# Optimization experiments

Measured on AMD Instinct MI355X. Metric: run time of the kernel, lower is better.

Reference implementation:

```python
import jax, jax.numpy as jnp
import numpy as np

H = 16
D = 1024
DH = D // H


def setup_inputs() -> dict:
    key = jax.random.key(0)
    ks = jax.random.split(key, 7)
    B, N = 4, 2048
    queries = jax.random.normal(ks[0], (B, N, D), dtype=jnp.float32)
    keys = jax.random.normal(ks[1], (B, N, D), dtype=jnp.float32)
    values = jax.random.normal(ks[2], (B, N, D), dtype=jnp.float32)
    s = 1.0 / np.sqrt(D)
    Wq = jax.random.normal(ks[3], (D, D), dtype=jnp.float32) * s
    Wk = jax.random.normal(ks[4], (D, D), dtype=jnp.float32) * s
    Wv = jax.random.normal(ks[5], (D, D), dtype=jnp.float32) * s
    Wo = jax.random.normal(ks[6], (D, D), dtype=jnp.float32) * s
    return {"queries": queries, "keys": keys, "values": values,
            "Wq": Wq, "Wk": Wk, "Wv": Wv, "Wo": Wo}


def reference(queries, keys, values, Wq, Wk, Wv, Wo):
    B, Nq, _ = queries.shape
    Nk = keys.shape[1]
    # torch Linear (no bias): y = x @ W.T
    q = (queries @ Wq.T).reshape(B, Nq, H, DH)
    k = (keys @ Wk.T).reshape(B, Nk, H, DH)
    v = (values @ Wv.T).reshape(B, Nk, H, DH)
    scale = 1.0 / jnp.sqrt(jnp.asarray(DH, dtype=q.dtype))
    scores = jnp.einsum("bqhd,bkhd->bhqk", q, k) * scale  # (B,H,Nq,Nk)
    attn = jax.nn.softmax(scores, axis=-1)
    ctx = jnp.einsum("bhqk,bkhd->bqhd", attn, v).reshape(B, Nq, D)
    return ctx @ Wo.T
```

## Files before the change

kernel.cpp:

```cpp
#include <hip/hip_runtime.h>
#include <hip/hip_bf16.h>
#include <stdint.h>

typedef short bf16x8 __attribute__((ext_vector_type(8)));
typedef float f32x4 __attribute__((ext_vector_type(4)));
typedef unsigned short u16;
typedef unsigned int u32;

#define MFMA(a, b, c) __builtin_amdgcn_mfma_f32_16x16x32_bf16(a, b, c, 0, 0, 0)

#if __has_builtin(__builtin_amdgcn_exp2f)
#define EXP2F(x) __builtin_amdgcn_exp2f(x)
#else
#define EXP2F(x) exp2f(x)
#endif
#if __has_builtin(__builtin_amdgcn_rcpf)
#define RCPF(x) __builtin_amdgcn_rcpf(x)
#else
#define RCPF(x) (1.0f / (x))
#endif

__device__ __forceinline__ u16 f2bf(float f) {
  u32 u = __builtin_bit_cast(u32, f);
  u += 0x7FFFu + ((u >> 16) & 1u);
  return (u16)(u >> 16);
}

__device__ __forceinline__ bf16x8 cvt8(const float* p) {
  const float4 f0 = *(const float4*)p;
  const float4 f1 = *(const float4*)(p + 4);
  bf16x8 r;
  r[0] = (short)f2bf(f0.x); r[1] = (short)f2bf(f0.y);
  r[2] = (short)f2bf(f0.z); r[3] = (short)f2bf(f0.w);
  r[4] = (short)f2bf(f1.x); r[5] = (short)f2bf(f1.y);
  r[6] = (short)f2bf(f1.z); r[7] = (short)f2bf(f1.w);
  return r;
}

__device__ __forceinline__ void async16(const u16* g, u16* l) {
  __builtin_amdgcn_global_load_lds(
      (const __attribute__((address_space(1))) void*)g,
      (__attribute__((address_space(3))) void*)l, 16, 0, 0);
}

__global__ __launch_bounds__(256) void cvt_qk(const float* __restrict__ xq,
                                              const float* __restrict__ xk,
                                              u16* __restrict__ dq,
                                              u16* __restrict__ dk) {
  int b = (int)blockIdx.x;
  const float* s;
  u16* d;
  if (b < 4096) { s = xq; d = dq; } else { s = xk; d = dk; b -= 4096; }
  const size_t off = (size_t)b * 2048 + (size_t)threadIdx.x * 8;
  *(bf16x8*)(d + off) = cvt8(s + off);
}

__global__ __launch_bounds__(256) void cvt_vw(
    const float* __restrict__ xv, const float* __restrict__ wq,
    const float* __restrict__ wk, const float* __restrict__ wv,
    const float* __restrict__ wo, u16* __restrict__ dv, u16* __restrict__ dwq,
    u16* __restrict__ dwk, u16* __restrict__ dwv, u16* __restrict__ dwo) {
  int b = (int)blockIdx.x;
  const float* s;
  u16* d;
  if (b < 4096) { s = xv; d = dv; }
  else if (b < 4608) { s = wq; d = dwq; b -= 4096; }
  else if (b < 5120) { s = wk; d = dwk; b -= 4608; }
  else if (b < 5632) { s = wv; d = dwv; b -= 5120; }
  else { s = wo; d = dwo; b -= 5632; }
  const size_t off = (size_t)b * 2048 + (size_t)threadIdx.x * 8;
  *(bf16x8*)(d + off) = cvt8(s + off);
}

__device__ __forceinline__ void gemm_core(const u16* __restrict__ A,
                                          const u16* __restrict__ W,
                                          u16* smA, u16* smB, f32x4 acc[4][4],
                                          int m0, int n0, int tid) {
  const int w = tid >> 6, l = tid & 63;
  const int la = l & 15, q = l >> 4;
  const int wm = w >> 1, wn = w & 1;
  const int srow = tid >> 3, sblk = tid & 7;

  for (int kk = 0; kk < 16; ++kk) {
    __syncthreads();
#pragma unroll
    for (int jj = 0; jj < 4; ++jj) {
      const int row = jj * 32 + srow;
      const int sb = (sblk ^ (row & 7)) * 8;
      const int ld = (jj * 256 + tid) * 8;
      async16(A + (size_t)(m0 + row) * 1024 + kk * 64 + sb, smA + ld);
      async16(W + (size_t)(n0 + row) * 1024 + kk * 64 + sb, smB + ld);
    }
    __syncthreads();
#pragma unroll
    for (int ks = 0; ks < 2; ++ks) {
      bf16x8 af[4], bfr[4];
#pragma unroll
      for (int im = 0; im < 4; ++im)
        af[im] = *(const bf16x8*)(smA + (wm * 64 + im * 16 + la) * 64 +
                                  (((ks * 4 + q) ^ (la & 7)) * 8));
#pragma unroll
      for (int in = 0; in < 4; ++in)
        bfr[in] = *(const bf16x8*)(smB + (wn * 64 + in * 16 + la) * 64 +
                                   (((ks * 4 + q) ^ (la & 7)) * 8));
#pragma unroll
      for (int im = 0; im < 4; ++im)
#pragma unroll
        for (int in = 0; in < 4; ++in)
          acc[im][in] = MFMA(af[im], bfr[in], acc[im][in]);
    }
  }
}

__global__ __launch_bounds__(256, 2) void gemm_qkv(
    const u16* __restrict__ Xqb, const u16* __restrict__ Xkb,
    const u16* __restrict__ Xvb, const u16* __restrict__ Wqb,
    const u16* __restrict__ Wkb, const u16* __restrict__ Wvb,
    u16* __restrict__ Qh, u16* __restrict__ Kh, u16* __restrict__ VTp) {
  __shared__ u16 smA[128 * 64];
  __shared__ u16 smB[128 * 64];
  const int z = (int)blockIdx.z;
  const u16* A = (z == 0) ? Xqb : (z == 1) ? Xkb : Xvb;
  const u16* W = (z == 0) ? Wqb : (z == 1) ? Wkb : Wvb;
  u16* out = (z == 0) ? Qh : (z == 1) ? Kh : VTp;
  const float scale = (z == 0) ? 0.18033688011112042f : 1.0f;

  const int tid = (int)threadIdx.x;
  const int w = tid >> 6, l = tid & 63;
  const int la = l & 15, q = l >> 4;
  const int m0 = blockIdx.x * 128, n0 = blockIdx.y * 128;
  const int wm = w >> 1, wn = w & 1;

  f32x4 acc[4][4];
#pragma unroll
  for (int i = 0; i < 4; ++i)
#pragma unroll
    for (int j = 0; j < 4; ++j) acc[i][j] = (f32x4){0.f, 0.f, 0.f, 0.f};

  gemm_core(A, W, smA, smB, acc, m0, n0, tid);

#pragma unroll
  for (int im = 0; im < 4; ++im) {
    const int mbase = m0 + wm * 64 + im * 16 + q * 4;
#pragma unroll
    for (int in = 0; in < 4; ++in) {
      const int n = n0 + wn * 64 + in * 16 + la;
      if (z == 2) {
        const int b = mbase >> 11, nr = mbase & 2047;
        const int h = n >> 6, d = n & 63;
        uint2 val;
        val.x = (u32)f2bf(acc[im][in][0]) | ((u32)f2bf(acc[im][in][1]) << 16);
        val.y = (u32)f2bf(acc[im][in][2]) | ((u32)f2bf(acc[im][in][3]) << 16);
        *(uint2*)(VTp + ((size_t)((b * 16 + h) * 64 + d)) * 2048 + nr) = val;
      } else {
#pragma unroll
        for (int r = 0; r < 4; ++r) {
          const int mm = mbase + r;
          const int b = mm >> 11, nr = mm & 2047;
          const int h = n >> 6, d = n & 63;
          out[((size_t)((b * 16 + h) * 2048 + nr)) * 64 + d] =
              f2bf(acc[im][in][r] * scale);
        }
      }
    }
  }
}

__global__ __launch_bounds__(256, 2) void gemm_out(const u16* __restrict__ A,
                                                   const u16* __restrict__ W,
                                                   float* __restrict__ out) {
  __shared__ u16 smA[128 * 64];
  __shared__ u16 smB[128 * 64];
  const int tid = (int)threadIdx.x;
  const int w = tid >> 6, l = tid & 63;
  const int la = l & 15, q = l >> 4;
  const int m0 = blockIdx.x * 128, n0 = blockIdx.y * 128;
  const int wm = w >> 1, wn = w & 1;

  f32x4 acc[4][4];
#pragma unroll
  for (int i = 0; i < 4; ++i)
#pragma unroll
    for (int j = 0; j < 4; ++j) acc[i][j] = (f32x4){0.f, 0.f, 0.f, 0.f};

  gemm_core(A, W, smA, smB, acc, m0, n0, tid);

#pragma unroll
  for (int im = 0; im < 4; ++im) {
    const int mbase = m0 + wm * 64 + im * 16 + q * 4;
#pragma unroll
    for (int in = 0; in < 4; ++in) {
      const int n = n0 + wn * 64 + in * 16 + la;
#pragma unroll
      for (int r = 0; r < 4; ++r)
        out[(size_t)(mbase + r) * 1024 + n] = acc[im][in][r];
    }
  }
}

__global__ __launch_bounds__(256, 2) void attn_kernel(const u16* __restrict__ Qh,
                                                      const u16* __restrict__ Kh,
                                                      const u16* __restrict__ VT,
                                                      u16* __restrict__ ctx) {
  __shared__ u16 smK[128 * 64];
  __shared__ u16 smV[64 * 128];
  __shared__ u16 smP[128 * 128];

  const int tid = (int)threadIdx.x;
  const int w = tid >> 6, l = tid & 63;
  const int la = l & 15, q = l >> 4;
  const int qt = blockIdx.x, bh = blockIdx.y;
  const u16* Qp = Qh + (size_t)bh * (2048 * 64);
  const u16* Kp = Kh + (size_t)bh * (2048 * 64);
  const u16* Vp = VT + (size_t)bh * (64 * 2048);

  bf16x8 qf[2][2];
#pragma unroll
  for (int ic = 0; ic < 2; ++ic)
#pragma unroll
    for (int ks = 0; ks < 2; ++ks)
      qf[ic][ks] = *(const bf16x8*)(Qp + (size_t)(qt * 128 + w * 32 + ic * 16 + la) * 64 +
                                    ks * 32 + q * 8);

  f32x4 accO[2][4];
#pragma unroll
  for (int ic = 0; ic < 2; ++ic)
#pragma unroll
    for (int dc = 0; dc < 4; ++dc) accO[ic][dc] = (f32x4){0.f, 0.f, 0.f, 0.f};
  float m_[2] = {-__builtin_inff(), -__builtin_inff()};
  float l_[2] = {0.f, 0.f};
  float alpha_[2];
  bool skip_[2];

  const int srow = tid >> 3, sblk = tid & 7;

  for (int kt = 0; kt < 16; ++kt) {
    __syncthreads();
#pragma unroll
    for (int jj = 0; jj < 4; ++jj) {
      const int idx = jj * 256 + tid;
      const int krow = jj * 32 + srow;
      const int ksb = (sblk ^ (krow & 7)) * 8;
      async16(Kp + (size_t)(kt * 128 + krow) * 64 + ksb, smK + idx * 8);
      const int vr = idx >> 4, vb = idx & 15;
      async16(Vp + (size_t)vr * 2048 + kt * 128 + ((vb ^ (vr & 15)) * 8),
              smV + idx * 8);
    }
    __syncthreads();

    f32x4 st[2][8];
#pragma unroll
    for (int ic = 0; ic < 2; ++ic)
#pragma unroll
      for (int jc = 0; jc < 8; ++jc) st[ic][jc] = (f32x4){0.f, 0.f, 0.f, 0.f};
    __builtin_amdgcn_s_setprio(1);
#pragma unroll
    for (int ks = 0; ks < 2; ++ks) {
      bf16x8 kf[8];
#pragma unroll
      for (int jc = 0; jc < 8; ++jc)
        kf[jc] = *(const bf16x8*)(smK + (jc * 16 + la) * 64 +
                                  (((ks * 4 + q) ^ (la & 7)) * 8));
#pragma unroll
      for (int jc = 0; jc < 8; ++jc)
#pragma unroll
        for (int ic = 0; ic < 2; ++ic)
          st[ic][jc] = MFMA(kf[jc], qf[ic][ks], st[ic][jc]);
    }
    __builtin_amdgcn_s_setprio(0);

#pragma unroll
    for (int ic = 0; ic < 2; ++ic) {
      float mx = -__builtin_inff();
#pragma unroll
      for (int jc = 0; jc < 8; ++jc)
#pragma unroll
        for (int r = 0; r < 4; ++r) mx = fmaxf(mx, st[ic][jc][r]);
      mx = fmaxf(mx, __shfl_xor(mx, 16));
      mx = fmaxf(mx, __shfl_xor(mx, 32));
      const bool skip = (bool)__all(mx - m_[ic] <= 8.0f);
      float mnew, al;
      if (skip) { mnew = m_[ic]; al = 1.0f; }
      else { mnew = fmaxf(m_[ic], mx); al = EXP2F(m_[ic] - mnew); }
      skip_[ic] = skip;
      alpha_[ic] = al;
      float rs = 0.f;
      const int i = w * 32 + ic * 16 + la;
#pragma unroll
      for (int jc = 0; jc < 8; ++jc) {
        const float p0 = EXP2F(st[ic][jc][0] - mnew);
        const float p1 = EXP2F(st[ic][jc][1] - mnew);
        const float p2 = EXP2F(st[ic][jc][2] - mnew);
        const float p3 = EXP2F(st[ic][jc][3] - mnew);
        rs += (p0 + p1) + (p2 + p3);
        uint2 val;
        val.x = (u32)f2bf(p0) | ((u32)f2bf(p1) << 16);
        val.y = (u32)f2bf(p2) | ((u32)f2bf(p3) << 16);
        const int blk = (jc * 2 + (q >> 1)) ^ la;
        *(uint2*)(smP + i * 128 + blk * 8 + (q & 1) * 4) = val;
      }
      rs += __shfl_xor(rs, 16);
      rs += __shfl_xor(rs, 32);
      m_[ic] = mnew;
      l_[ic] = l_[ic] * alpha_[ic] + rs;
    }
    __syncthreads();

#pragma unroll
    for (int ic = 0; ic < 2; ++ic)
      if (!skip_[ic]) {
#pragma unroll
        for (int r = 0; r < 4; ++r) {
          const float a = __shfl(alpha_[ic], q * 4 + r);
#pragma unroll
          for (int dc = 0; dc < 4; ++dc) accO[ic][dc][r] *= a;
        }
      }

#pragma unroll
    for (int ks = 0; ks < 4; ++ks) {
      bf16x8 pf[2], vf[4];
#pragma unroll
      for (int ic = 0; ic < 2; ++ic)
        pf[ic] = *(const bf16x8*)(smP + (w * 32 + ic * 16 + la) * 128 +
                                  (((ks * 4 + q) ^ la) * 8));
#pragma unroll
      for (int dc = 0; dc < 4; ++dc)
        vf[dc] = *(const bf16x8*)(smV + (dc * 16 + la) * 128 +
                                  (((ks * 4 + q) ^ la) * 8));
      __builtin_amdgcn_s_setprio(1);
#pragma unroll
      for (int ic = 0; ic < 2; ++ic)
#pragma unroll
        for (int dc = 0; dc < 4; ++dc)
          accO[ic][dc] = MFMA(pf[ic], vf[dc], accO[ic][dc]);
      __builtin_amdgcn_s_setprio(0);
    }
  }

  const int b = bh >> 4, h = bh & 15;
#pragma unroll
  for (int ic = 0; ic < 2; ++ic)
#pragma unroll
    for (int r = 0; r < 4; ++r) {
      const float inv = RCPF(__shfl(l_[ic], q * 4 + r));
      const size_t rowoff =
          ((size_t)(b * 2048 + qt * 128 + w * 32 + ic * 16 + q * 4 + r)) * 1024 + h * 64;
#pragma unroll
      for (int dc = 0; dc < 4; ++dc)
        ctx[rowoff + dc * 16 + la] = f2bf(accO[ic][dc][r] * inv);
    }
}

extern "C" void kernel_launch(void* const* d_in, const int* in_sizes, int n_in,
                              void* d_out, int out_size, void* d_ws, size_t ws_size,
                              hipStream_t stream) {
  const float* Xq = (const float*)d_in[0];
  const float* Xk = (const float*)d_in[1];
  const float* Xv = (const float*)d_in[2];
  const float* Wq = (const float*)d_in[3];
  const float* Wk = (const float*)d_in[4];
  const float* Wv = (const float*)d_in[5];
  const float* Wo = (const float*)d_in[6];

  const size_t T = 8388608;
  const size_t WN = 1048576;
  u16 *Xqb, *Xkb, *Xvb, *Wqb, *Wkb, *Wvb, *Wob, *Qh, *Kh, *VTp, *ctx;
  if (ws_size >= (7 * T + 4 * WN) * sizeof(u16)) {
    u16* ws = (u16*)d_ws;
    Xqb = ws; Xkb = ws + T; Xvb = ws + 2 * T;
    Qh = ws + 3 * T; Kh = ws + 4 * T; VTp = ws + 5 * T; ctx = ws + 6 * T;
    Wqb = ws + 7 * T; Wkb = Wqb + WN; Wvb = Wkb + WN; Wob = Wvb + WN;
  } else {
    u16* ob = (u16*)d_out;
    u16* bq = (u16*)d_in[0];
    u16* bk = (u16*)d_in[1];
    u16* bv = (u16*)d_in[2];
    Xqb = ob; Xkb = ob + T;
    Xvb = bq; Wqb = bq + T; Wkb = Wqb + WN; Wvb = Wkb + WN; Wob = Wvb + WN;
    Qh = bk; Kh = bk + T;
    VTp = bv; ctx = bv + T;
  }

  dim3 blk(256);
  hipLaunchKernelGGL(cvt_qk, dim3(8192), blk, 0, stream, Xq, Xk, Xqb, Xkb);
  hipLaunchKernelGGL(cvt_vw, dim3(6144), blk, 0, stream, Xv, Wq, Wk, Wv, Wo,
                     Xvb, Wqb, Wkb, Wvb, Wob);
  hipLaunchKernelGGL(gemm_qkv, dim3(64, 8, 3), blk, 0, stream, Xqb, Xkb, Xvb,
                     Wqb, Wkb, Wvb, Qh, Kh, VTp);
  hipLaunchKernelGGL(attn_kernel, dim3(16, 64), blk, 0, stream, Qh, Kh, VTp, ctx);
  hipLaunchKernelGGL(gemm_out, dim3(64, 8), blk, 0, stream, ctx, Wob, (float*)d_out);
}
```

Baseline: 362.0 us.

## Double-buffer LDS tiles in GEMMs and attention to overlap loads with MFMA

The GEMM core now uses two LDS buffers for A and W and issues the async global-to-LDS loads for the next K tile before computing on the current one, which removes one barrier per iteration. The attention kernel double-buffers V and prefetches the next K and V tiles after the softmax barrier, so they load during the PV matmul. The bf16 conversion also switches to the compiler's native __bf16 cast. LDS use per block grows (GEMM from 32KB to 64KB, attention adds 16KB), which may lower occupancy under the launch bounds of 2 blocks. Correctness relies on the async loads completing by the next barrier.

```diff
diff --git a/kernel.cpp b/kernel.cpp
--- a/kernel.cpp
+++ b/kernel.cpp
@@ -21,9 +21,7 @@
 #endif
 
 __device__ __forceinline__ u16 f2bf(float f) {
-  u32 u = __builtin_bit_cast(u32, f);
-  u += 0x7FFFu + ((u >> 16) & 1u);
-  return (u16)(u >> 16);
+  return __builtin_bit_cast(u16, static_cast<__bf16>(f));
 }
 
 __device__ __forceinline__ bf16x8 cvt8(const float* p) {
@@ -72,43 +70,63 @@
   *(bf16x8*)(d + off) = cvt8(s + off);
 }
 
+__device__ __forceinline__ void stage_gemm(const u16* __restrict__ A,
+                                           const u16* __restrict__ W,
+                                           u16* smA, u16* smB, int m0, int n0,
+                                           int kk, int tid) {
+  const int srow = tid >> 3, sblk = tid & 7;
+#pragma unroll
+  for (int jj = 0; jj < 4; ++jj) {
+    const int row = jj * 32 + srow;
+    const int sb = (sblk ^ (row & 7)) * 8;
+    const int ld = (jj * 256 + tid) * 8;
+    async16(A + (size_t)(m0 + row) * 1024 + kk * 64 + sb, smA + ld);
+    async16(W + (size_t)(n0 + row) * 1024 + kk * 64 + sb, smB + ld);
+  }
+}
+
+__device__ __forceinline__ void gemm_compute(const u16* smA, const u16* smB,
+                                             f32x4 acc[4][4], int wm, int wn,
+                                             int la, int q) {
+#pragma unroll
+  for (int ks = 0; ks < 2; ++ks) {
+    bf16x8 af[4], bfr[4];
+#pragma unroll
+    for (int im = 0; im < 4; ++im)
+      af[im] = *(const bf16x8*)(smA + (wm * 64 + im * 16 + la) * 64 +
+                                (((ks * 4 + q) ^ (la & 7)) * 8));
+#pragma unroll
+    for (int in = 0; in < 4; ++in)
+      bfr[in] = *(const bf16x8*)(smB + (wn * 64 + in * 16 + la) * 64 +
+                                 (((ks * 4 + q) ^ (la & 7)) * 8));
+#pragma unroll
+    for (int im = 0; im < 4; ++im)
+#pragma unroll
+      for (int in = 0; in < 4; ++in)
+        acc[im][in] = MFMA(af[im], bfr[in], acc[im][in]);
+  }
+}
+
 __device__ __forceinline__ void gemm_core(const u16* __restrict__ A,
                                           const u16* __restrict__ W,
-                                          u16* smA, u16* smB, f32x4 acc[4][4],
-                                          int m0, int n0, int tid) {
+                                          u16* smA0, u16* smB0, u16* smA1,
+                                          u16* smB1, f32x4 acc[4][4], int m0,
+                                          int n0, int tid) {
   const int w = tid >> 6, l = tid & 63;
   const int la = l & 15, q = l >> 4;
   const int wm = w >> 1, wn = w & 1;
-  const int srow = tid >> 3, sblk = tid & 7;
-
+
+  stage_gemm(A, W, smA0, smB0, m0, n0, 0, tid);
+  __syncthreads();
+#pragma unroll 2
   for (int kk = 0; kk < 16; ++kk) {
+    u16* ca = (kk & 1) ? smA1 : smA0;
+    u16* cb = (kk & 1) ? smB1 : smB0;
+    u16* na = (kk & 1) ? smA0 : smA1;
+    u16* nb = (kk & 1) ? smB0 : smB1;
+    if (kk < 15) stage_gemm(A, W, na, nb, m0, n0, kk + 1, tid);
+    gemm_compute(ca, cb, acc, wm, wn, la, q);
     __syncthreads();
-#pragma unroll
-    for (int jj = 0; jj < 4; ++jj) {
-      const int row = jj * 32 + srow;
-      const int sb = (sblk ^ (row & 7)) * 8;
-      const int ld = (jj * 256 + tid) * 8;
-      async16(A + (size_t)(m0 + row) * 1024 + kk * 64 + sb, smA + ld);
-      async16(W + (size_t)(n0 + row) * 1024 + kk * 64 + sb, smB + ld);
-    }
-    __syncthreads();
-#pragma unroll
-    for (int ks = 0; ks < 2; ++ks) {
-      bf16x8 af[4], bfr[4];
-#pragma unroll
-      for (int im = 0; im < 4; ++im)
-        af[im] = *(const bf16x8*)(smA + (wm * 64 + im * 16 + la) * 64 +
-                                  (((ks * 4 + q) ^ (la & 7)) * 8));
-#pragma unroll
-      for (int in = 0; in < 4; ++in)
-        bfr[in] = *(const bf16x8*)(smB + (wn * 64 + in * 16 + la) * 64 +
-                                   (((ks * 4 + q) ^ (la & 7)) * 8));
-#pragma unroll
-      for (int im = 0; im < 4; ++im)
-#pragma unroll
-        for (int in = 0; in < 4; ++in)
-          acc[im][in] = MFMA(af[im], bfr[in], acc[im][in]);
-    }
   }
 }
 
@@ -117,8 +135,8 @@
     const u16* __restrict__ Xvb, const u16* __restrict__ Wqb,
     const u16* __restrict__ Wkb, const u16* __restrict__ Wvb,
     u16* __restrict__ Qh, u16* __restrict__ Kh, u16* __restrict__ VTp) {
-  __shared__ u16 smA[128 * 64];
-  __shared__ u16 smB[128 * 64];
+  __shared__ u16 smA0[128 * 64], smB0[128 * 64];
+  __shared__ u16 smA1[128 * 64], smB1[128 * 64];
   const int z = (int)blockIdx.z;
   const u16* A = (z == 0) ? Xqb : (z == 1) ? Xkb : Xvb;
   const u16* W = (z == 0) ? Wqb : (z == 1) ? Wkb : Wvb;
@@ -137,7 +155,7 @@
 #pragma unroll
     for (int j = 0; j < 4; ++j) acc[i][j] = (f32x4){0.f, 0.f, 0.f, 0.f};
 
-  gemm_core(A, W, smA, smB, acc, m0, n0, tid);
+  gemm_core(A, W, smA0, smB0, smA1, smB1, acc, m0, n0, tid);
 
 #pragma unroll
   for (int im = 0; im < 4; ++im) {
@@ -169,8 +187,8 @@
 __global__ __launch_bounds__(256, 2) void gemm_out(const u16* __restrict__ A,
                                                    const u16* __restrict__ W,
                                                    float* __restrict__ out) {
-  __shared__ u16 smA[128 * 64];
-  __shared__ u16 smB[128 * 64];
+  __shared__ u16 smA0[128 * 64], smB0[128 * 64];
+  __shared__ u16 smA1[128 * 64], smB1[128 * 64];
   const int tid = (int)threadIdx.x;
   const int w = tid >> 6, l = tid & 63;
   const int la = l & 15, q = l >> 4;
@@ -183,7 +201,7 @@
 #pragma unroll
     for (int j = 0; j < 4; ++j) acc[i][j] = (f32x4){0.f, 0.f, 0.f, 0.f};
 
-  gemm_core(A, W, smA, smB, acc, m0, n0, tid);
+  gemm_core(A, W, smA0, smB0, smA1, smB1, acc, m0, n0, tid);
 
 #pragma unroll
   for (int im = 0; im < 4; ++im) {
@@ -203,7 +221,8 @@
                                                       const u16* __restrict__ VT,
                                                       u16* __restrict__ ctx) {
   __shared__ u16 smK[128 * 64];
-  __shared__ u16 smV[64 * 128];
+  __shared__ u16 smV0[64 * 128];
+  __shared__ u16 smV1[64 * 128];
   __shared__ u16 smP[128 * 128];
 
   const int tid = (int)threadIdx.x;
@@ -234,18 +253,30 @@
 
   const int srow = tid >> 3, sblk = tid & 7;
 
-  for (int kt = 0; kt < 16; ++kt) {
-    __syncthreads();
+  auto stageK = [&](int kt) {
+#pragma unroll
+    for (int jj = 0; jj < 4; ++jj) {
+      const int krow = jj * 32 + srow;
+      const int ksb = (sblk ^ (krow & 7)) * 8;
+      async16(Kp + (size_t)(kt * 128 + krow) * 64 + ksb, smK + (jj * 256 + tid) * 8);
+    }
+  };
+  auto stageV = [&](int kt, u16* dst) {
 #pragma unroll
     for (int jj = 0; jj < 4; ++jj) {
       const int idx = jj * 256 + tid;
-      const int krow = jj * 32 + srow;
-      const int ksb = (sblk ^ (krow & 7)) * 8;
-      async16(Kp + (size_t)(kt * 128 + krow) * 64 + ksb, smK + idx * 8);
       const int vr = idx >> 4, vb = idx & 15;
       async16(Vp + (size_t)vr * 2048 + kt * 128 + ((vb ^ (vr & 15)) * 8),
-              smV + idx * 8);
-    }
+              dst + idx * 8);
+    }
+  };
+
+  stageK(0);
+  stageV(0, smV0);
+
+  for (int kt = 0; kt < 16; ++kt) {
+    u16* vcur = (kt & 1) ? smV1 : smV0;
+    u16* vnxt = (kt & 1) ? smV0 : smV1;
     __syncthreads();
 
     f32x4 st[2][8];
@@ -306,6 +337,11 @@
     }
     __syncthreads();
 
+    if (kt < 15) {
+      stageK(kt + 1);
+      stageV(kt + 1, vnxt);
+    }
+
 #pragma unroll
     for (int ic = 0; ic < 2; ++ic)
       if (!skip_[ic]) {
@@ -326,7 +362,7 @@
                                   (((ks * 4 + q) ^ la) * 8));
 #pragma unroll
       for (int dc = 0; dc < 4; ++dc)
-        vf[dc] = *(const bf16x8*)(smV + (dc * 16 + la) * 128 +
+        vf[dc] = *(const bf16x8*)(vcur + (dc * 16 + la) * 128 +
                                   (((ks * 4 + q) ^ la) * 8));
       __builtin_amdgcn_s_setprio(1);
 #pragma unroll
```

After: 338.2 us. 1.07x faster.
